# Kernel tuning notes

Measured on AMD Instinct MI355X. Metric: run time of the kernel, lower is better.

The kernel has to match this reference:

```python
import jax, jax.numpy as jnp
import numpy as np
from functools import partial

H = 768          # hidden_size (bert-base)
S = 256          # seq_len, forced by pool Linear(256*H -> H)
V = 30522        # vocab_size
NUM_TAGS = 2
B = 32


def _lstm_layer(x, w_ih, w_hh, b_ih, b_hh):
    # x: (B, S, I); torch weight layout: w_ih (4H, I), w_hh (4H, H), gate order i,f,g,o
    b, _, _ = x.shape
    h0 = jnp.zeros((b, H), x.dtype)
    c0 = jnp.zeros((b, H), x.dtype)
    bias = b_ih + b_hh

    def step(carry, xt):
        h, c = carry
        gates = xt @ w_ih.T + h @ w_hh.T + bias          # (B, 4H)
        i, f, g, o = jnp.split(gates, 4, axis=-1)
        i = jax.nn.sigmoid(i)
        f = jax.nn.sigmoid(f)
        g = jnp.tanh(g)
        o = jax.nn.sigmoid(o)
        c = f * c + i * g
        h = o * jnp.tanh(c)
        return (h, c), h

    _, hs = jax.lax.scan(step, (h0, c0), x.transpose(1, 0, 2))  # hs: (S, B, H)
    return hs.transpose(1, 0, 2)


def setup_inputs() -> dict:
    key = jax.random.key(0)
    ks = jax.random.split(key, 16)
    sc = 0.02
    inp = {
        "input_ids": jax.random.randint(ks[0], (B, S), 0, V, dtype=jnp.int32),
        "attention_mask": jnp.ones((B, S), jnp.int32),
        "token_type_ids": jnp.zeros((B, S), jnp.int32),
        "seq_label": jax.random.randint(ks[1], (B, NUM_TAGS), 0, 2, dtype=jnp.int32),
        "entity_ids": jax.random.randint(ks[2], (B, S), 0, 2, dtype=jnp.int32),
        "embed_table": jax.random.normal(ks[3], (V, H), jnp.float32) * sc,
        "w_ih0": jax.random.normal(ks[4], (4 * H, H), jnp.float32) * sc,
        "w_hh0": jax.random.normal(ks[5], (4 * H, H), jnp.float32) * sc,
        "b_ih0": jnp.zeros((4 * H,), jnp.float32),
        "b_hh0": jnp.zeros((4 * H,), jnp.float32),
        "w_ih1": jax.random.normal(ks[6], (4 * H, H), jnp.float32) * sc,
        "w_hh1": jax.random.normal(ks[7], (4 * H, H), jnp.float32) * sc,
        "b_ih1": jnp.zeros((4 * H,), jnp.float32),
        "b_hh1": jnp.zeros((4 * H,), jnp.float32),
        "pool_w": jax.random.normal(ks[8], (S * H, H), jnp.float32) * 0.002,
        "pool_b": jnp.zeros((H,), jnp.float32),
        "lin_w": jax.random.normal(ks[9], (H, NUM_TAGS), jnp.float32) * sc,
        "lin_b": jnp.zeros((NUM_TAGS,), jnp.float32),
    }
    return inp


def reference(input_ids, attention_mask, token_type_ids, seq_label, entity_ids,
              embed_table, w_ih0, w_hh0, b_ih0, b_hh0, w_ih1, w_hh1, b_ih1, b_hh1,
              pool_w, pool_b, lin_w, lin_b):
    x = embed_table[input_ids]                              # (B, S, H)
    out = _lstm_layer(x, w_ih0, w_hh0, b_ih0, b_hh0)        # layer 1
    out = _lstm_layer(out, w_ih1, w_hh1, b_ih1, b_hh1)      # layer 2 -> (B, S, H)

    seq_out = out.reshape(out.shape[0], -1) @ pool_w + pool_b   # (B, H)

    # batched version of the per-sample loop:
    # entity_out = tokens * (entity_ids == 1); concat seq_out row; global max over tokens
    mask = (entity_ids == 1).astype(out.dtype)[:, :, None]      # (B, S, 1)
    entity_out = out * mask                                     # (B, S, H)
    batch_out = jnp.maximum(entity_out.max(axis=1), seq_out)    # adaptive_max_pool1d(size=1)

    logits = batch_out @ lin_w + lin_b                          # (B, num_tags)

    # BCEWithLogitsLoss (dropout in eval mode = identity), numerically stable
    y = seq_label.astype(logits.dtype)
    loss = jnp.mean(jnp.maximum(logits, 0) - logits * y + jnp.log1p(jnp.exp(-jnp.abs(logits))))
    return (loss, logits)
```

## Files before the change

### kernel.cpp

```cpp
#include <hip/hip_runtime.h>
#include <hip/hip_bf16.h>
#include <stdint.h>

constexpr int Hh  = 768;
constexpr int Ss  = 256;
constexpr int Bb  = 32;
constexpr int G4  = 4 * Hh;
constexpr int MR  = Bb * Ss;
constexpr int NWGL = 96;
constexpr int UPW8 = Hh / NWGL;
constexpr int LCW  = 4 * UPW8;
constexpr int WPAD = Hh + 8;
constexpr int CPT  = 256;
constexpr int PB   = 40;
constexpr int NCH  = 3;

typedef short bf16x8 __attribute__((ext_vector_type(8)));
typedef float f32x4  __attribute__((ext_vector_type(4)));
typedef float f32x2  __attribute__((ext_vector_type(2)));
typedef uint32_t u32x4 __attribute__((ext_vector_type(4)));

__device__ __forceinline__ unsigned short f2bf(float f) {
  union { float f; uint32_t u; } v; v.f = f;
  uint32_t u = v.u;
  return (unsigned short)((u + 0x7FFFu + ((u >> 16) & 1u)) >> 16);
}
__device__ __forceinline__ float bf2f(unsigned short h) {
  union { uint32_t u; float f; } v; v.u = ((uint32_t)h) << 16; return v.f;
}

__global__ __launch_bounds__(256) void k_embed(const int* __restrict__ ids,
                                               const float* __restrict__ table,
                                               unsigned short* __restrict__ x_bf) {
  int row = blockIdx.x;
  int id  = ids[row];
  const float* src = table + (size_t)id * Hh;
  unsigned short* dst = x_bf + (size_t)row * Hh;
  for (int j = threadIdx.x; j < Hh; j += 256) dst[j] = f2bf(src[j]);
}

__global__ __launch_bounds__(256) void k_cast(const float* __restrict__ src,
                                              unsigned short* __restrict__ dst, int n4) {
  int i = blockIdx.x * 256 + threadIdx.x;
  if (i < n4) {
    float4 v = ((const float4*)src)[i];
    uint2 o;
    o.x = (uint32_t)f2bf(v.x) | ((uint32_t)f2bf(v.y) << 16);
    o.y = (uint32_t)f2bf(v.z) | ((uint32_t)f2bf(v.w) << 16);
    ((uint2*)dst)[i] = o;
  }
}

__global__ __launch_bounds__(256) void k_gemm_bt(const unsigned short* __restrict__ A,
                                                 const unsigned short* __restrict__ Bw,
                                                 unsigned short* __restrict__ g2,
                                                 const float* __restrict__ bias1,
                                                 const float* __restrict__ bias2,
                                                 int M, int N, int K) {
  constexpr int BM = 128, BN = 128, BK = 64;
  __shared__ unsigned short Asm[BM * BK];
  __shared__ unsigned short Bsm[BN * BK];
  const int tid = threadIdx.x, lane = tid & 63, wave = tid >> 6;
  const int m0 = blockIdx.x * BM, n0 = blockIdx.y * BN;
  const int wm = (wave & 1) * 64, wn = (wave >> 1) * 64;

  f32x4 acc[4][4];
  #pragma unroll
  for (int a = 0; a < 4; ++a)
    #pragma unroll
    for (int b = 0; b < 4; ++b) acc[a][b] = (f32x4){0.f, 0.f, 0.f, 0.f};

  const int nk = K / BK;
  bf16x8 ar[4], br[4];
  #pragma unroll
  for (int r = 0; r < 4; ++r) {
    int fb = r * 4096 + tid * 16;
    int row = fb >> 7;
    int kb  = (fb >> 4) & 7;
    ar[r] = *(const bf16x8*)(A  + (size_t)(m0 + row) * K + kb * 8);
    br[r] = *(const bf16x8*)(Bw + (size_t)(n0 + row) * K + kb * 8);
  }
  for (int it = 0; it < nk; ++it) {
    __syncthreads();
    #pragma unroll
    for (int r = 0; r < 4; ++r) {
      int fb = r * 4096 + tid * 16;
      int row = fb >> 7;
      int kb  = (fb >> 4) & 7;
      int sb  = kb ^ (row & 7);
      *(bf16x8*)((char*)Asm + row * 128 + sb * 16) = ar[r];
      *(bf16x8*)((char*)Bsm + row * 128 + sb * 16) = br[r];
    }
    __syncthreads();
    if (it + 1 < nk) {
      int k0 = (it + 1) * BK;
      #pragma unroll
      for (int r = 0; r < 4; ++r) {
        int fb = r * 4096 + tid * 16;
        int row = fb >> 7;
        int kb  = (fb >> 4) & 7;
        ar[r] = *(const bf16x8*)(A  + (size_t)(m0 + row) * K + k0 + kb * 8);
        br[r] = *(const bf16x8*)(Bw + (size_t)(n0 + row) * K + k0 + kb * 8);
      }
    }
    #pragma unroll
    for (int kk = 0; kk < 2; ++kk) {
      bf16x8 af[4], bfr[4];
      #pragma unroll
      for (int mi = 0; mi < 4; ++mi) {
        int row = wm + mi * 16 + (lane & 15);
        int kb  = kk * 4 + (lane >> 4);
        int sb  = kb ^ (row & 7);
        af[mi] = *(const bf16x8*)((const char*)Asm + row * 128 + sb * 16);
      }
      #pragma unroll
      for (int ni = 0; ni < 4; ++ni) {
        int row = wn + ni * 16 + (lane & 15);
        int kb  = kk * 4 + (lane >> 4);
        int sb  = kb ^ (row & 7);
        bfr[ni] = *(const bf16x8*)((const char*)Bsm + row * 128 + sb * 16);
      }
      #pragma unroll
      for (int mi = 0; mi < 4; ++mi)
        #pragma unroll
        for (int ni = 0; ni < 4; ++ni)
          acc[mi][ni] = __builtin_amdgcn_mfma_f32_16x16x32_bf16(af[mi], bfr[ni], acc[mi][ni], 0, 0, 0);
    }
  }
  #pragma unroll
  for (int mi = 0; mi < 4; ++mi)
    #pragma unroll
    for (int ni = 0; ni < 4; ++ni)
      #pragma unroll
      for (int r = 0; r < 4; ++r) {
        int row = m0 + wm + mi * 16 + (lane >> 4) * 4 + r;
        int n   = n0 + wn + ni * 16 + (lane & 15);
        int bb = row >> 8, ss = row & 255;
        int gi = n / Hh, u = n - gi * Hh;
        int wg = u >> 3, lc = gi * 8 + (u & 7);
        float v = acc[mi][ni][r] + bias1[n] + bias2[n];
        g2[(((size_t)ss * NWGL + wg) * Bb + bb) * LCW + lc] = f2bf(v);
      }
}

__global__ __launch_bounds__(256) void k_lstm2(
    const unsigned short* __restrict__ g2,
    const unsigned short* __restrict__ w_hh0b,
    const unsigned short* __restrict__ w_ih1b,
    const unsigned short* __restrict__ w_hh1b,
    const float* __restrict__ b_ih1,
    const float* __restrict__ b_hh1,
    unsigned short* __restrict__ hseq1,
    unsigned short* __restrict__ hseq2,
    unsigned int* __restrict__ sync) {
  __shared__ __align__(16) unsigned short Whh[LCW * WPAD];
  __shared__ __align__(16) unsigned short Wih[LCW * WPAD];
  __shared__ __align__(16) unsigned short hbuf[2][16][8];
  __shared__ __align__(16) float gsum[2][2][16][33];
  __shared__ int prodf[2], consf[2];

  const int wgid = blockIdx.x;
  const int tid = threadIdx.x;
  const int lane = tid & 63, w = tid >> 6;
  unsigned int* cnt1 = sync;
  unsigned int* cnt2 = sync + Ss * CPT;

  const int layer = wgid >= NWGL;
  const int wg = layer ? wgid - NWGL : wgid;
  const int u0 = wg * UPW8;
  const int bkt = wg & 15;

  if (tid < 2) { prodf[tid] = 0; consf[tid] = -1; }

  {
    const unsigned short* src = layer ? w_hh1b : w_hh0b;
    for (int cch = tid; cch < LCW * 96; cch += 256) {
      int row = cch / 96, kc = cch - row * 96;
      int gi = row >> 3, u = row & 7;
      *(bf16x8*)&Whh[row * WPAD + kc * 8] =
          *(const bf16x8*)(src + (size_t)(gi * Hh + u0 + u) * Hh + kc * 8);
    }
    if (layer) {
      for (int cch = tid; cch < LCW * 96; cch += 256) {
        int row = cch / 96, kc = cch - row * 96;
        int gi = row >> 3, u = row & 7;
        *(bf16x8*)&Wih[row * WPAD + kc * 8] =
            *(const bf16x8*)(w_ih1b + (size_t)(gi * Hh + u0 + u) * Hh + kc * 8);
      }
    }
  }
  __syncthreads();

  const int l15 = lane & 15, kq = lane >> 4;
  const bool lo8 = (l15 < 8);

  if (layer && w >= 2) {
    const int bh = w - 2;
    const int brow = bh * 16 + l15;
    for (int t = 0; t < Ss; ++t) {
      {
        const unsigned int* b1 = cnt1 + (size_t)t * CPT;
        for (;;) {
          unsigned v = 12;
          if (lane < 16)
            v = __hip_atomic_load(b1 + lane * 16, __ATOMIC_RELAXED, __HIP_MEMORY_SCOPE_AGENT);
          if (__all(v >= 12u)) break;
          __builtin_amdgcn_s_sleep(1);
        }
        asm volatile("" ::: "memory");
      }
      const unsigned short* ap = hseq1 + ((size_t)t * Bb + brow) * Hh + kq * 8;
      bf16x8 areg[24];
      #pragma unroll
      for (int kk = 0; kk < 24; ++kk) areg[kk] = *(const bf16x8*)(ap + kk * 32);
      f32x4 aI[2][2];
      #pragma unroll
      for (int nt = 0; nt < 2; ++nt) {
        aI[nt][0] = (f32x4){0.f,0.f,0.f,0.f}; aI[nt][1] = (f32x4){0.f,0.f,0.f,0.f};
        const int c = nt * 16 + l15;
        #pragma unroll
        for (int kk = 0; kk < 24; ++kk) {
          bf16x8 bfr = *(const bf16x8*)&Wih[c * WPAD + kk * 32 + kq * 8];
          aI[nt][kk & 1] = __builtin_amdgcn_mfma_f32_16x16x32_bf16(areg[kk], bfr, aI[nt][kk & 1], 0, 0, 0);
        }
      }
      while (__hip_atomic_load(&consf[bh], __ATOMIC_RELAXED, __HIP_MEMORY_SCOPE_WORKGROUP) < t - 1)
        __builtin_amdgcn_s_sleep(0);
      const int par = t & 1;
      #pragma unroll
      for (int nt = 0; nt < 2; ++nt)
        #pragma unroll
        for (int r = 0; r < 4; ++r)
          gsum[par][bh][kq * 4 + r][nt * 16 + l15] = aI[nt][0][r] + aI[nt][1][r];
      __hip_atomic_store(&prodf[bh], t + 1, __ATOMIC_RELEASE, __HIP_MEMORY_SCOPE_WORKGROUP);
    }
    return;
  }
  if (!layer && w >= 2) return;

  const int bh = w;
  const int brow = bh * 16 + l15;
  const float k1 = lo8 ? 2.f : 1.f;
  const float m1 = lo8 ? 2.f : 1.f;
  const float d1 = lo8 ? -1.f : 0.f;

  float bl[2] = {0.f, 0.f};
  if (layer) {
    #pragma unroll
    for (int nt = 0; nt < 2; ++nt) {
      int c = nt * 16 + l15;
      int gcol = (c >> 3) * Hh + u0 + (c & 7);
      bl[nt] = b_ih1[gcol] + b_hh1[gcol];
    }
  }
  unsigned short gc[2][4];
  if (!layer) {
    const unsigned short* grow = g2 + ((size_t)0 * NWGL + wg) * (Bb * LCW);
    #pragma unroll
    for (int nt = 0; nt < 2; ++nt)
      #pragma unroll
      for (int r = 0; r < 4; ++r)
        gc[nt][r] = grow[(bh * 16 + kq * 4 + r) * LCW + nt * 16 + l15];
  }
  float cc[4] = {0.f, 0.f, 0.f, 0.f};
  unsigned short* hout = layer ? hseq2 : hseq1;
  unsigned int* mycnt = layer ? cnt2 : cnt1;

  for (int t = 0; t < Ss; ++t) {
    f32x4 aW[2][2];
    #pragma unroll
    for (int nt = 0; nt < 2; ++nt) {
      aW[nt][0] = (f32x4){0.f,0.f,0.f,0.f}; aW[nt][1] = (f32x4){0.f,0.f,0.f,0.f};
    }
    if (t > 0) {
      {
        const unsigned int* bown = mycnt + (size_t)(t - 1) * CPT;
        for (;;) {
          unsigned v = 12;
          if (lane < 16)
            v = __hip_atomic_load(bown + lane * 16, __ATOMIC_RELAXED, __HIP_MEMORY_SCOPE_AGENT);
          if (__all(v >= 12u)) break;
          __builtin_amdgcn_s_sleep(1);
        }
        asm volatile("" ::: "memory");
      }
      const unsigned short* ap = hout + ((size_t)(t - 1) * Bb + brow) * Hh + kq * 8;
      bf16x8 areg[24];
      #pragma unroll
      for (int kk = 0; kk < 24; ++kk) areg[kk] = *(const bf16x8*)(ap + kk * 32);
      #pragma unroll
      for (int nt = 0; nt < 2; ++nt) {
        const int c = nt * 16 + l15;
        #pragma unroll
        for (int kk = 0; kk < 24; ++kk) {
          bf16x8 bfr = *(const bf16x8*)&Whh[c * WPAD + kk * 32 + kq * 8];
          aW[nt][kk & 1] = __builtin_amdgcn_mfma_f32_16x16x32_bf16(areg[kk], bfr, aW[nt][kk & 1], 0, 0, 0);
        }
      }
    }

    float gin[2][4];
    if (layer) {
      while (__hip_atomic_load(&prodf[bh], __ATOMIC_ACQUIRE, __HIP_MEMORY_SCOPE_WORKGROUP) < t + 1)
        __builtin_amdgcn_s_sleep(0);
      const int par = t & 1;
      #pragma unroll
      for (int nt = 0; nt < 2; ++nt)
        #pragma unroll
        for (int r = 0; r < 4; ++r)
          gin[nt][r] = gsum[par][bh][kq * 4 + r][nt * 16 + l15] + bl[nt];
      __hip_atomic_store(&consf[bh], t, __ATOMIC_RELEASE, __HIP_MEMORY_SCOPE_WORKGROUP);
    } else {
      #pragma unroll
      for (int nt = 0; nt < 2; ++nt)
        #pragma unroll
        for (int r = 0; r < 4; ++r)
          gin[nt][r] = bf2f(gc[nt][r]);
    }

    float act0[4], act1[4];
    #pragma unroll
    for (int r = 0; r < 4; ++r) {
      float v0 = aW[0][0][r] + aW[0][1][r] + gin[0][r];
      act0[r] = 1.f / (1.f + __expf(-v0));
      float v1 = aW[1][0][r] + aW[1][1][r] + gin[1][r];
      act1[r] = m1 / (1.f + __expf(-k1 * v1)) + d1;
    }

    #pragma unroll
    for (int r = 0; r < 4; ++r) {
      float p0 = __shfl_xor(act0[r], 8);
      float p1 = __shfl_xor(act1[r], 8);
      float iv = lo8 ? act0[r] : p0;
      float fv = lo8 ? p0 : act0[r];
      float gv = lo8 ? act1[r] : p1;
      float ov = lo8 ? p1 : act1[r];
      float cn = fv * cc[r] + iv * gv;
      cc[r] = cn;
      float e = __expf(-2.f * cn);
      float hv = ov * (1.f - e) / (1.f + e);
      if (lo8) hbuf[w][kq * 4 + r][l15] = f2bf(hv);
    }
    asm volatile("s_waitcnt lgkmcnt(0)" ::: "memory");

    if (lane < 16) {
      const unsigned long long* hb = (const unsigned long long*)&hbuf[w][lane][0];
      unsigned long long x0 = hb[0], x1 = hb[1];
      unsigned long long* hp =
          (unsigned long long*)(hout + ((size_t)t * Bb + (bh * 16 + lane)) * Hh + u0);
      __hip_atomic_store(hp + 0, x0, __ATOMIC_RELAXED, __HIP_MEMORY_SCOPE_AGENT);
      __hip_atomic_store(hp + 1, x1, __ATOMIC_RELAXED, __HIP_MEMORY_SCOPE_AGENT);
    }
    asm volatile("s_waitcnt vmcnt(0)" ::: "memory");
    if (lane == 0) {
      unsigned int* cp = mycnt + (size_t)t * CPT + bkt * 16;
      (void)__hip_atomic_fetch_add(cp, 1u, __ATOMIC_RELAXED, __HIP_MEMORY_SCOPE_AGENT);
    }

    if (!layer && t + 1 < Ss) {
      const unsigned short* grow = g2 + ((size_t)(t + 1) * NWGL + wg) * (Bb * LCW);
      #pragma unroll
      for (int nt = 0; nt < 2; ++nt)
        #pragma unroll
        for (int r = 0; r < 4; ++r)
          gc[nt][r] = grow[(bh * 16 + kq * 4 + r) * LCW + nt * 16 + l15];
    }
  }
}

__global__ __launch_bounds__(256) void k_pool_partial(const unsigned short* __restrict__ hseq2,
                                                      const float* __restrict__ pw,
                                                      float* __restrict__ partial) {
  __shared__ __align__(16) unsigned short osm[Hh * PB];
  const int tid = threadIdx.x;
  const int s = blockIdx.x, nc = blockIdx.y;
  for (int b = 0; b < Bb; ++b) {
    const unsigned short* src = hseq2 + ((size_t)s * Bb + b) * Hh;
    for (int k = tid; k < Hh; k += 256) osm[k * PB + b] = src[k];
  }
  __syncthreads();
  f32x2 acc[16];
  #pragma unroll
  for (int bp = 0; bp < 16; ++bp) acc[bp] = (f32x2){0.f, 0.f};
  const float* pbase = pw + (size_t)s * Hh * Hh + nc * 256 + tid;
  #pragma unroll 4
  for (int k = 0; k < Hh; ++k) {
    float wv = pbase[(size_t)k * Hh];
    u32x4 h0 = *(const u32x4*)&osm[k * PB + 0];
    u32x4 h1 = *(const u32x4*)&osm[k * PB + 8];
    u32x4 h2 = *(const u32x4*)&osm[k * PB + 16];
    u32x4 h3 = *(const u32x4*)&osm[k * PB + 24];
    uint32_t hw[16] = {h0[0],h0[1],h0[2],h0[3], h1[0],h1[1],h1[2],h1[3],
                       h2[0],h2[1],h2[2],h2[3], h3[0],h3[1],h3[2],h3[3]};
    #pragma unroll
    for (int bp = 0; bp < 16; ++bp) {
      uint32_t pv = hw[bp];
      f32x2 ov;
      ov.x = __uint_as_float(pv << 16);
      ov.y = __uint_as_float(pv & 0xffff0000u);
      acc[bp] += ov * wv;
    }
  }
  float* pout = partial + (size_t)(s * NCH + nc) * (Bb * 256);
  #pragma unroll
  for (int bp = 0; bp < 16; ++bp) {
    pout[(size_t)(bp * 2 + 0) * 256 + tid] = acc[bp].x;
    pout[(size_t)(bp * 2 + 1) * 256 + tid] = acc[bp].y;
  }
}

__global__ __launch_bounds__(256) void k_pool_reduce(const float* __restrict__ partial,
                                                     const float* __restrict__ pool_b,
                                                     float* __restrict__ seq_out) {
  int i = blockIdx.x * 256 + threadIdx.x;
  int b = i / Hh, n = i - b * Hh;
  int nchunk = n >> 8, nn = n & 255;
  float acc = pool_b[n];
  const float* p = partial + (size_t)nchunk * (Bb * 256) + b * 256 + nn;
  #pragma unroll 8
  for (int t = 0; t < Ss; ++t) acc += p[(size_t)t * NCH * (Bb * 256)];
  seq_out[i] = acc;
}

__global__ __launch_bounds__(256) void k_entity_logits(const unsigned short* __restrict__ hseq2,
                                                       const float* __restrict__ seq_out,
                                                       const int* __restrict__ entity_ids,
                                                       const float* __restrict__ lin_w,
                                                       const float* __restrict__ lin_b,
                                                       float* __restrict__ logits_ws,
                                                       float* __restrict__ dlogits) {
  const int b = blockIdx.x, tid = threadIdx.x;
  float m0 = -1e30f, m1 = -1e30f, m2 = -1e30f;
  for (int s = 0; s < Ss; ++s) {
    bool e = entity_ids[b * Ss + s] == 1;
    const unsigned short* row = hseq2 + ((size_t)s * Bb + b) * Hh;
    float v0 = bf2f(row[tid]);
    float v1 = bf2f(row[256 + tid]);
    float v2 = bf2f(row[512 + tid]);
    v0 = e ? v0 : 0.f; v1 = e ? v1 : 0.f; v2 = e ? v2 : 0.f;
    m0 = fmaxf(m0, v0); m1 = fmaxf(m1, v1); m2 = fmaxf(m2, v2);
  }
  __shared__ float red[512];
  float p0 = 0.f, p1 = 0.f;
  float mm[3] = {m0, m1, m2};
  #pragma unroll
  for (int j = 0; j < 3; ++j) {
    int n = j * 256 + tid;
    float bo = fmaxf(mm[j], seq_out[b * Hh + n]);
    p0 += bo * lin_w[n * 2 + 0];
    p1 += bo * lin_w[n * 2 + 1];
  }
  red[tid] = p0; red[256 + tid] = p1;
  __syncthreads();
  for (int off = 128; off > 0; off >>= 1) {
    if (tid < off) { red[tid] += red[tid + off]; red[256 + tid] += red[256 + tid + off]; }
    __syncthreads();
  }
  if (tid == 0) {
    float l0 = red[0] + lin_b[0], l1 = red[256] + lin_b[1];
    logits_ws[b * 2] = l0; logits_ws[b * 2 + 1] = l1;
    dlogits[b * 2] = l0;  dlogits[b * 2 + 1] = l1;
  }
}

__global__ void k_loss(const float* __restrict__ logits, const int* __restrict__ lab,
                       float* __restrict__ dout) {
  __shared__ float red[64];
  int i = threadIdx.x;
  float l = logits[i];
  float y = (float)lab[i];
  red[i] = fmaxf(l, 0.f) - l * y + log1pf(__expf(-fabsf(l)));
  __syncthreads();
  for (int off = 32; off > 0; off >>= 1) {
    if (i < off) red[i] += red[i + off];
    __syncthreads();
  }
  if (i == 0) dout[0] = red[0] * (1.f / 64.f);
}

extern "C" void kernel_launch(void* const* d_in, const int* in_sizes, int n_in,
                              void* d_out, int out_size, void* d_ws, size_t ws_size,
                              hipStream_t stream) {
  const int*   input_ids  = (const int*)d_in[0];
  const int*   seq_label  = (const int*)d_in[3];
  const int*   entity_ids = (const int*)d_in[4];
  const float* embed      = (const float*)d_in[5];
  const float* w_ih0      = (const float*)d_in[6];
  const float* w_hh0      = (const float*)d_in[7];
  const float* b_ih0      = (const float*)d_in[8];
  const float* b_hh0      = (const float*)d_in[9];
  const float* w_ih1      = (const float*)d_in[10];
  const float* w_hh1      = (const float*)d_in[11];
  const float* b_ih1      = (const float*)d_in[12];
  const float* b_hh1      = (const float*)d_in[13];
  const float* pool_w     = (const float*)d_in[14];
  const float* pool_b     = (const float*)d_in[15];
  const float* lin_w      = (const float*)d_in[16];
  const float* lin_b      = (const float*)d_in[17];
  float* out = (float*)d_out;

  const size_t SZ_XO = (size_t)Bb * Ss * Hh * 2;
  const size_t SZ_W  = (size_t)G4 * Hh * 2;
  const size_t SZ_G  = (size_t)Bb * Ss * G4 * 2;
  const size_t SZ_SY = (size_t)2 * Ss * CPT * 4;
  char* ws = (char*)d_ws;
  size_t off = 0;
  unsigned short* x_bf   = (unsigned short*)(ws + off); off += SZ_XO;
  unsigned short* wb_ih0 = (unsigned short*)(ws + off); off += SZ_W;
  unsigned short* wb_hh0 = (unsigned short*)(ws + off); off += SZ_W;
  unsigned short* wb_ih1 = (unsigned short*)(ws + off); off += SZ_W;
  unsigned short* wb_hh1 = (unsigned short*)(ws + off); off += SZ_W;
  unsigned short* g2     = (unsigned short*)(ws + off); off += SZ_G;
  unsigned short* hseq1  = (unsigned short*)(ws + off); off += SZ_XO;
  unsigned short* hseq2  = (unsigned short*)(ws + off); off += SZ_XO;
  float*          seq_out= (float*)(ws + off);          off += (size_t)Bb * Hh * 4;
  float*          logits = (float*)(ws + off);          off += 1024;
  unsigned int*   syncb  = (unsigned int*)(ws + off);   off += SZ_SY;
  float*          partial = (float*)ws;

  hipMemsetAsync(syncb, 0, SZ_SY, stream);

  k_embed<<<Bb * Ss, 256, 0, stream>>>(input_ids, embed, x_bf);
  int n4 = (G4 * Hh) / 4;
  int cgrid = (n4 + 255) / 256;
  k_cast<<<cgrid, 256, 0, stream>>>(w_ih0, wb_ih0, n4);
  k_cast<<<cgrid, 256, 0, stream>>>(w_hh0, wb_hh0, n4);
  k_cast<<<cgrid, 256, 0, stream>>>(w_ih1, wb_ih1, n4);
  k_cast<<<cgrid, 256, 0, stream>>>(w_hh1, wb_hh1, n4);

  dim3 ggrid(MR / 128, G4 / 128);
  k_gemm_bt<<<ggrid, 256, 0, stream>>>(x_bf, wb_ih0, g2, b_ih0, b_hh0, MR, G4, Hh);

  k_lstm2<<<2 * NWGL, 256, 0, stream>>>(g2, wb_hh0, wb_ih1, wb_hh1,
                                        b_ih1, b_hh1, hseq1, hseq2, syncb);

  dim3 pgrid(Ss, NCH);
  k_pool_partial<<<pgrid, 256, 0, stream>>>(hseq2, pool_w, partial);
  k_pool_reduce<<<(Bb * Hh) / 256, 256, 0, stream>>>(partial, pool_b, seq_out);
  k_entity_logits<<<Bb, 256, 0, stream>>>(hseq2, seq_out, entity_ids, lin_w, lin_b,
                                          logits, out + 1);
  k_loss<<<1, 64, 0, stream>>>(logits, seq_label, out);
}
```

Measured before the change: 2.290 ms.

## Fuse layer-0 input projection into persistent LSTM kernel, drop separate GEMM and casts

Removes the standalone bf16 weight-cast kernels and the big x·W_ih0 GEMM, so the layer-0 workgroups compute their input projection per timestep using the two spare waves already used by layer 1. Weights are now cast from fp32 to bf16 directly while being loaded into LDS. The embedding output is stored time-major to match. Cross-workgroup polling is reduced to one wave per workgroup, which then signals the other waves through an LDS flag. This avoids the large g2 intermediate write and read plus several launches, but adds per-step input-projection work to layer 0 inside the recurrent loop.

```diff
diff --git a/kernel.cpp b/kernel.cpp
--- a/kernel.cpp
+++ b/kernel.cpp
@@ -5,8 +5,6 @@
 constexpr int Hh  = 768;
 constexpr int Ss  = 256;
 constexpr int Bb  = 32;
-constexpr int G4  = 4 * Hh;
-constexpr int MR  = Bb * Ss;
 constexpr int NWGL = 96;
 constexpr int UPW8 = Hh / NWGL;
 constexpr int LCW  = 4 * UPW8;
@@ -33,123 +31,19 @@
                                                const float* __restrict__ table,
                                                unsigned short* __restrict__ x_bf) {
   int row = blockIdx.x;
+  int b = row / Ss, s = row - b * Ss;
   int id  = ids[row];
   const float* src = table + (size_t)id * Hh;
-  unsigned short* dst = x_bf + (size_t)row * Hh;
+  unsigned short* dst = x_bf + ((size_t)s * Bb + b) * Hh;
   for (int j = threadIdx.x; j < Hh; j += 256) dst[j] = f2bf(src[j]);
 }
 
-__global__ __launch_bounds__(256) void k_cast(const float* __restrict__ src,
-                                              unsigned short* __restrict__ dst, int n4) {
-  int i = blockIdx.x * 256 + threadIdx.x;
-  if (i < n4) {
-    float4 v = ((const float4*)src)[i];
-    uint2 o;
-    o.x = (uint32_t)f2bf(v.x) | ((uint32_t)f2bf(v.y) << 16);
-    o.y = (uint32_t)f2bf(v.z) | ((uint32_t)f2bf(v.w) << 16);
-    ((uint2*)dst)[i] = o;
-  }
-}
-
-__global__ __launch_bounds__(256) void k_gemm_bt(const unsigned short* __restrict__ A,
-                                                 const unsigned short* __restrict__ Bw,
-                                                 unsigned short* __restrict__ g2,
-                                                 const float* __restrict__ bias1,
-                                                 const float* __restrict__ bias2,
-                                                 int M, int N, int K) {
-  constexpr int BM = 128, BN = 128, BK = 64;
-  __shared__ unsigned short Asm[BM * BK];
-  __shared__ unsigned short Bsm[BN * BK];
-  const int tid = threadIdx.x, lane = tid & 63, wave = tid >> 6;
-  const int m0 = blockIdx.x * BM, n0 = blockIdx.y * BN;
-  const int wm = (wave & 1) * 64, wn = (wave >> 1) * 64;
-
-  f32x4 acc[4][4];
-  #pragma unroll
-  for (int a = 0; a < 4; ++a)
-    #pragma unroll
-    for (int b = 0; b < 4; ++b) acc[a][b] = (f32x4){0.f, 0.f, 0.f, 0.f};
-
-  const int nk = K / BK;
-  bf16x8 ar[4], br[4];
-  #pragma unroll
-  for (int r = 0; r < 4; ++r) {
-    int fb = r * 4096 + tid * 16;
-    int row = fb >> 7;
-    int kb  = (fb >> 4) & 7;
-    ar[r] = *(const bf16x8*)(A  + (size_t)(m0 + row) * K + kb * 8);
-    br[r] = *(const bf16x8*)(Bw + (size_t)(n0 + row) * K + kb * 8);
-  }
-  for (int it = 0; it < nk; ++it) {
-    __syncthreads();
-    #pragma unroll
-    for (int r = 0; r < 4; ++r) {
-      int fb = r * 4096 + tid * 16;
-      int row = fb >> 7;
-      int kb  = (fb >> 4) & 7;
-      int sb  = kb ^ (row & 7);
-      *(bf16x8*)((char*)Asm + row * 128 + sb * 16) = ar[r];
-      *(bf16x8*)((char*)Bsm + row * 128 + sb * 16) = br[r];
-    }
-    __syncthreads();
-    if (it + 1 < nk) {
-      int k0 = (it + 1) * BK;
-      #pragma unroll
-      for (int r = 0; r < 4; ++r) {
-        int fb = r * 4096 + tid * 16;
-        int row = fb >> 7;
-        int kb  = (fb >> 4) & 7;
-        ar[r] = *(const bf16x8*)(A  + (size_t)(m0 + row) * K + k0 + kb * 8);
-        br[r] = *(const bf16x8*)(Bw + (size_t)(n0 + row) * K + k0 + kb * 8);
-      }
-    }
-    #pragma unroll
-    for (int kk = 0; kk < 2; ++kk) {
-      bf16x8 af[4], bfr[4];
-      #pragma unroll
-      for (int mi = 0; mi < 4; ++mi) {
-        int row = wm + mi * 16 + (lane & 15);
-        int kb  = kk * 4 + (lane >> 4);
-        int sb  = kb ^ (row & 7);
-        af[mi] = *(const bf16x8*)((const char*)Asm + row * 128 + sb * 16);
-      }
-      #pragma unroll
-      for (int ni = 0; ni < 4; ++ni) {
-        int row = wn + ni * 16 + (lane & 15);
-        int kb  = kk * 4 + (lane >> 4);
-        int sb  = kb ^ (row & 7);
-        bfr[ni] = *(const bf16x8*)((const char*)Bsm + row * 128 + sb * 16);
-      }
-      #pragma unroll
-      for (int mi = 0; mi < 4; ++mi)
-        #pragma unroll
-        for (int ni = 0; ni < 4; ++ni)
-          acc[mi][ni] = __builtin_amdgcn_mfma_f32_16x16x32_bf16(af[mi], bfr[ni], acc[mi][ni], 0, 0, 0);
-    }
-  }
-  #pragma unroll
-  for (int mi = 0; mi < 4; ++mi)
-    #pragma unroll
-    for (int ni = 0; ni < 4; ++ni)
-      #pragma unroll
-      for (int r = 0; r < 4; ++r) {
-        int row = m0 + wm + mi * 16 + (lane >> 4) * 4 + r;
-        int n   = n0 + wn + ni * 16 + (lane & 15);
-        int bb = row >> 8, ss = row & 255;
-        int gi = n / Hh, u = n - gi * Hh;
-        int wg = u >> 3, lc = gi * 8 + (u & 7);
-        float v = acc[mi][ni][r] + bias1[n] + bias2[n];
-        g2[(((size_t)ss * NWGL + wg) * Bb + bb) * LCW + lc] = f2bf(v);
-      }
-}
-
 __global__ __launch_bounds__(256) void k_lstm2(
-    const unsigned short* __restrict__ g2,
-    const unsigned short* __restrict__ w_hh0b,
-    const unsigned short* __restrict__ w_ih1b,
-    const unsigned short* __restrict__ w_hh1b,
-    const float* __restrict__ b_ih1,
-    const float* __restrict__ b_hh1,
+    const unsigned short* __restrict__ x_bf,
+    const float* __restrict__ w_ih0, const float* __restrict__ w_hh0,
+    const float* __restrict__ w_ih1, const float* __restrict__ w_hh1,
+    const float* __restrict__ b_ih0, const float* __restrict__ b_hh0,
+    const float* __restrict__ b_ih1, const float* __restrict__ b_hh1,
     unsigned short* __restrict__ hseq1,
     unsigned short* __restrict__ hseq2,
     unsigned int* __restrict__ sync) {
@@ -158,6 +52,7 @@
   __shared__ __align__(16) unsigned short hbuf[2][16][8];
   __shared__ __align__(16) float gsum[2][2][16][33];
   __shared__ int prodf[2], consf[2];
+  __shared__ int stepC, stepP;
 
   const int wgid = blockIdx.x;
   const int tid = threadIdx.x;
@@ -171,45 +66,64 @@
   const int bkt = wg & 15;
 
   if (tid < 2) { prodf[tid] = 0; consf[tid] = -1; }
+  if (tid == 2) stepC = 0;
+  if (tid == 3) stepP = 0;
 
   {
-    const unsigned short* src = layer ? w_hh1b : w_hh0b;
+    const float* whsrc = layer ? w_hh1 : w_hh0;
+    const float* wisrc = layer ? w_ih1 : w_ih0;
     for (int cch = tid; cch < LCW * 96; cch += 256) {
       int row = cch / 96, kc = cch - row * 96;
       int gi = row >> 3, u = row & 7;
-      *(bf16x8*)&Whh[row * WPAD + kc * 8] =
-          *(const bf16x8*)(src + (size_t)(gi * Hh + u0 + u) * Hh + kc * 8);
-    }
-    if (layer) {
-      for (int cch = tid; cch < LCW * 96; cch += 256) {
-        int row = cch / 96, kc = cch - row * 96;
-        int gi = row >> 3, u = row & 7;
-        *(bf16x8*)&Wih[row * WPAD + kc * 8] =
-            *(const bf16x8*)(w_ih1b + (size_t)(gi * Hh + u0 + u) * Hh + kc * 8);
-      }
+      const float* sp = whsrc + ((size_t)gi * Hh + u0 + u) * Hh + kc * 8;
+      float4 va = ((const float4*)sp)[0], vb = ((const float4*)sp)[1];
+      bf16x8 pk;
+      pk[0] = (short)f2bf(va.x); pk[1] = (short)f2bf(va.y);
+      pk[2] = (short)f2bf(va.z); pk[3] = (short)f2bf(va.w);
+      pk[4] = (short)f2bf(vb.x); pk[5] = (short)f2bf(vb.y);
+      pk[6] = (short)f2bf(vb.z); pk[7] = (short)f2bf(vb.w);
+      *(bf16x8*)&Whh[row * WPAD + kc * 8] = pk;
+      const float* sp2 = wisrc + ((size_t)gi * Hh + u0 + u) * Hh + kc * 8;
+      float4 vc = ((const float4*)sp2)[0], vd = ((const float4*)sp2)[1];
+      bf16x8 pk2;
+      pk2[0] = (short)f2bf(vc.x); pk2[1] = (short)f2bf(vc.y);
+      pk2[2] = (short)f2bf(vc.z); pk2[3] = (short)f2bf(vc.w);
+      pk2[4] = (short)f2bf(vd.x); pk2[5] = (short)f2bf(vd.y);
+      pk2[6] = (short)f2bf(vd.z); pk2[7] = (short)f2bf(vd.w);
+      *(bf16x8*)&Wih[row * WPAD + kc * 8] = pk2;
     }
   }
   __syncthreads();
 
   const int l15 = lane & 15, kq = lane >> 4;
   const bool lo8 = (l15 < 8);
-
-  if (layer && w >= 2) {
+  volatile int* scp = &stepC;
+  volatile int* spp = &stepP;
+
+  if (w >= 2) {
     const int bh = w - 2;
     const int brow = bh * 16 + l15;
     for (int t = 0; t < Ss; ++t) {
-      {
-        const unsigned int* b1 = cnt1 + (size_t)t * CPT;
-        for (;;) {
-          unsigned v = 12;
-          if (lane < 16)
-            v = __hip_atomic_load(b1 + lane * 16, __ATOMIC_RELAXED, __HIP_MEMORY_SCOPE_AGENT);
-          if (__all(v >= 12u)) break;
-          __builtin_amdgcn_s_sleep(1);
+      if (layer) {
+        if (w == 2) {
+          const unsigned int* bk = cnt1 + (size_t)t * CPT;
+          for (;;) {
+            unsigned v = 12;
+            if (lane < 16)
+              v = __hip_atomic_load(bk + lane * 16, __ATOMIC_RELAXED, __HIP_MEMORY_SCOPE_AGENT);
+            if (__all(v >= 12u)) break;
+            __builtin_amdgcn_s_sleep(2);
+          }
+          asm volatile("" ::: "memory");
+          if (lane == 0) *spp = t + 1;
+          asm volatile("s_waitcnt lgkmcnt(0)" ::: "memory");
+        } else {
+          while (*spp < t + 1) __builtin_amdgcn_s_sleep(1);
+          asm volatile("" ::: "memory");
         }
-        asm volatile("" ::: "memory");
       }
-      const unsigned short* ap = hseq1 + ((size_t)t * Bb + brow) * Hh + kq * 8;
+      const unsigned short* ap = (layer ? hseq1 : x_bf)
+                               + ((size_t)t * Bb + brow) * Hh + kq * 8;
       bf16x8 areg[24];
       #pragma unroll
       for (int kk = 0; kk < 24; ++kk) areg[kk] = *(const bf16x8*)(ap + kk * 32);
@@ -236,7 +150,6 @@
     }
     return;
   }
-  if (!layer && w >= 2) return;
 
   const int bh = w;
   const int brow = bh * 16 + l15;
@@ -244,24 +157,14 @@
   const float m1 = lo8 ? 2.f : 1.f;
   const float d1 = lo8 ? -1.f : 0.f;
 
-  float bl[2] = {0.f, 0.f};
-  if (layer) {
-    #pragma unroll
-    for (int nt = 0; nt < 2; ++nt) {
-      int c = nt * 16 + l15;
-      int gcol = (c >> 3) * Hh + u0 + (c & 7);
-      bl[nt] = b_ih1[gcol] + b_hh1[gcol];
-    }
-  }
-  unsigned short gc[2][4];
-  if (!layer) {
-    const unsigned short* grow = g2 + ((size_t)0 * NWGL + wg) * (Bb * LCW);
-    #pragma unroll
-    for (int nt = 0; nt < 2; ++nt)
-      #pragma unroll
-      for (int r = 0; r < 4; ++r)
-        gc[nt][r] = grow[(bh * 16 + kq * 4 + r) * LCW + nt * 16 + l15];
-  }
+  float bl[2];
+  #pragma unroll
+  for (int nt = 0; nt < 2; ++nt) {
+    int c = nt * 16 + l15;
+    int gcol = (c >> 3) * Hh + u0 + (c & 7);
+    bl[nt] = layer ? (b_ih1[gcol] + b_hh1[gcol]) : (b_ih0[gcol] + b_hh0[gcol]);
+  }
+
   float cc[4] = {0.f, 0.f, 0.f, 0.f};
   unsigned short* hout = layer ? hseq2 : hseq1;
   unsigned int* mycnt = layer ? cnt2 : cnt1;
@@ -273,15 +176,20 @@
       aW[nt][0] = (f32x4){0.f,0.f,0.f,0.f}; aW[nt][1] = (f32x4){0.f,0.f,0.f,0.f};
     }
     if (t > 0) {
-      {
+      if (w == 0) {
         const unsigned int* bown = mycnt + (size_t)(t - 1) * CPT;
         for (;;) {
           unsigned v = 12;
           if (lane < 16)
             v = __hip_atomic_load(bown + lane * 16, __ATOMIC_RELAXED, __HIP_MEMORY_SCOPE_AGENT);
           if (__all(v >= 12u)) break;
-          __builtin_amdgcn_s_sleep(1);
+          __builtin_amdgcn_s_sleep(2);
         }
+        asm volatile("" ::: "memory");
+        if (lane == 0) *scp = t;
+        asm volatile("s_waitcnt lgkmcnt(0)" ::: "memory");
+      } else {
+        while (*scp < t) __builtin_amdgcn_s_sleep(1);
         asm volatile("" ::: "memory");
       }
       const unsigned short* ap = hout + ((size_t)(t - 1) * Bb + brow) * Hh + kq * 8;
@@ -300,7 +208,7 @@
     }
 
     float gin[2][4];
-    if (layer) {
+    {
       while (__hip_atomic_load(&prodf[bh], __ATOMIC_ACQUIRE, __HIP_MEMORY_SCOPE_WORKGROUP) < t + 1)
         __builtin_amdgcn_s_sleep(0);
       const int par = t & 1;
@@ -310,12 +218,6 @@
         for (int r = 0; r < 4; ++r)
           gin[nt][r] = gsum[par][bh][kq * 4 + r][nt * 16 + l15] + bl[nt];
       __hip_atomic_store(&consf[bh], t, __ATOMIC_RELEASE, __HIP_MEMORY_SCOPE_WORKGROUP);
-    } else {
-      #pragma unroll
-      for (int nt = 0; nt < 2; ++nt)
-        #pragma unroll
-        for (int r = 0; r < 4; ++r)
-          gin[nt][r] = bf2f(gc[nt][r]);
     }
 
     float act0[4], act1[4];
@@ -355,15 +257,6 @@
     if (lane == 0) {
       unsigned int* cp = mycnt + (size_t)t * CPT + bkt * 16;
       (void)__hip_atomic_fetch_add(cp, 1u, __ATOMIC_RELAXED, __HIP_MEMORY_SCOPE_AGENT);
-    }
-
-    if (!layer && t + 1 < Ss) {
-      const unsigned short* grow = g2 + ((size_t)(t + 1) * NWGL + wg) * (Bb * LCW);
-      #pragma unroll
-      for (int nt = 0; nt < 2; ++nt)
-        #pragma unroll
-        for (int r = 0; r < 4; ++r)
-          gc[nt][r] = grow[(bh * 16 + kq * 4 + r) * LCW + nt * 16 + l15];
     }
   }
 }
@@ -500,17 +393,10 @@
   float* out = (float*)d_out;
 
   const size_t SZ_XO = (size_t)Bb * Ss * Hh * 2;
-  const size_t SZ_W  = (size_t)G4 * Hh * 2;
-  const size_t SZ_G  = (size_t)Bb * Ss * G4 * 2;
   const size_t SZ_SY = (size_t)2 * Ss * CPT * 4;
   char* ws = (char*)d_ws;
   size_t off = 0;
   unsigned short* x_bf   = (unsigned short*)(ws + off); off += SZ_XO;
-  unsigned short* wb_ih0 = (unsigned short*)(ws + off); off += SZ_W;
-  unsigned short* wb_hh0 = (unsigned short*)(ws + off); off += SZ_W;
-  unsigned short* wb_ih1 = (unsigned short*)(ws + off); off += SZ_W;
-  unsigned short* wb_hh1 = (unsigned short*)(ws + off); off += SZ_W;
-  unsigned short* g2     = (unsigned short*)(ws + off); off += SZ_G;
   unsigned short* hseq1  = (unsigned short*)(ws + off); off += SZ_XO;
   unsigned short* hseq2  = (unsigned short*)(ws + off); off += SZ_XO;
   float*          seq_out= (float*)(ws + off);          off += (size_t)Bb * Hh * 4;
@@ -521,18 +407,10 @@
   hipMemsetAsync(syncb, 0, SZ_SY, stream);
 
   k_embed<<<Bb * Ss, 256, 0, stream>>>(input_ids, embed, x_bf);
-  int n4 = (G4 * Hh) / 4;
-  int cgrid = (n4 + 255) / 256;
-  k_cast<<<cgrid, 256, 0, stream>>>(w_ih0, wb_ih0, n4);
-  k_cast<<<cgrid, 256, 0, stream>>>(w_hh0, wb_hh0, n4);
-  k_cast<<<cgrid, 256, 0, stream>>>(w_ih1, wb_ih1, n4);
-  k_cast<<<cgrid, 256, 0, stream>>>(w_hh1, wb_hh1, n4);
-
-  dim3 ggrid(MR / 128, G4 / 128);
-  k_gemm_bt<<<ggrid, 256, 0, stream>>>(x_bf, wb_ih0, g2, b_ih0, b_hh0, MR, G4, Hh);
-
-  k_lstm2<<<2 * NWGL, 256, 0, stream>>>(g2, wb_hh0, wb_ih1, wb_hh1,
-                                        b_ih1, b_hh1, hseq1, hseq2, syncb);
+
+  k_lstm2<<<2 * NWGL, 256, 0, stream>>>(x_bf, w_ih0, w_hh0, w_ih1, w_hh1,
+                                        b_ih0, b_hh0, b_ih1, b_hh1,
+                                        hseq1, hseq2, syncb);
 
   dim3 pgrid(Ss, NCH);
   k_pool_partial<<<pgrid, 256, 0, stream>>>(hseq2, pool_w, partial);
```

Measured after the change: 2.193 ms, median of 3. 4.2% less time.
